# Kernel optimization log

Measured on AMD Instinct MI355X. Metric: run time of the kernel, lower is better.

The kernel has to match this reference:

```python
import jax, jax.numpy as jnp
import numpy as np

D = 1024
H = 16
HD = D // H
SCALE = HD ** -0.5


def setup_inputs() -> dict:
    key = jax.random.key(0)
    ks = jax.random.split(key, 5)
    x = jax.random.normal(ks[0], (2, 2048, D), dtype=jnp.float32)
    s = 1.0 / np.sqrt(D)
    W_qkv = jax.random.uniform(ks[1], (D, 3 * D), jnp.float32, -s, s)
    b_qkv = jax.random.uniform(ks[2], (3 * D,), jnp.float32, -s, s)
    W_out = jax.random.uniform(ks[3], (D, D), jnp.float32, -s, s)
    b_out = jax.random.uniform(ks[4], (D,), jnp.float32, -s, s)
    return {"x": x, "W_qkv": W_qkv, "b_qkv": b_qkv, "W_out": W_out, "b_out": b_out}


def reference(x, W_qkv, b_qkv, W_out, b_out):
    B, S, _ = x.shape
    qkv = x @ W_qkv + b_qkv                       # [B,S,3D]
    qkv = qkv.reshape(B, S, 3, H, HD)
    q, k, v = jnp.moveaxis(qkv, 2, 0)             # each [B,S,H,HD]
    # scores: [B,H,S,S]
    scores = jnp.einsum("bshd,bthd->bhst", q, k) * SCALE
    attn = jax.nn.softmax(scores, axis=-1)        # dropout is identity in eval mode
    out = jnp.einsum("bhst,bthd->bshd", attn, v)  # [B,S,H,HD]
    out = out.reshape(B, S, H * HD)
    return out @ W_out + b_out
```

## Files before the change

### kernel.cpp

```cpp
#include <hip/hip_runtime.h>

typedef unsigned short u16;
typedef unsigned int   u32;

using short8 = __attribute__((ext_vector_type(8))) short;
using f32x4  = __attribute__((ext_vector_type(4))) float;
using half4  = __attribute__((ext_vector_type(4))) _Float16;
using half8  = __attribute__((ext_vector_type(8))) _Float16;

#define QSCALE 0.18033688011112042f
#define SXR(r) ((((r) ^ ((r) >> 2))) & 3)

__device__ __forceinline__ u16 f2bf(float f) {
  u32 u = __float_as_uint(f);
  return (u16)((u + 0x8000u) >> 16);
}
__device__ __forceinline__ u16 f2h(float f) {
  _Float16 h = (_Float16)f;
  return __builtin_bit_cast(u16, h);
}

__device__ __forceinline__ void gld16(const u16* g, u16* l) {
  __builtin_amdgcn_global_load_lds(
      (const __attribute__((address_space(1))) unsigned int*)g,
      (__attribute__((address_space(3))) unsigned int*)l, 16, 0, 0);
}

__global__ __launch_bounds__(256) void prep(
    const float* __restrict__ x, u16* __restrict__ x_bf,
    const float* __restrict__ Wq, u16* __restrict__ wq_t,
    const float* __restrict__ Wo, u16* __restrict__ wo_t) {
  __shared__ u32 s[32][33];
  const int bid = blockIdx.x, tid = threadIdx.x;
  if (bid < 4096) {
    int idx = bid * 256 + tid;
    float4 v = reinterpret_cast<const float4*>(x)[idx];
    ushort4 o;
    o.x = f2bf(v.x); o.y = f2bf(v.y); o.z = f2bf(v.z); o.w = f2bf(v.w);
    reinterpret_cast<ushort4*>(x_bf)[idx] = o;
    return;
  }
  const float* in; u16* out; int R, C, bx, by;
  if (bid < 7168) { int b = bid - 4096; in = Wq; out = wq_t; R = 1024; C = 3072; bx = b % 96; by = b / 96; }
  else            { int b = bid - 7168; in = Wo; out = wo_t; R = 1024; C = 1024; bx = b % 32; by = b / 32; }
  int c0 = bx * 32, r0 = by * 32;
  int j = tid & 31, i0 = tid >> 5;
#pragma unroll
  for (int p = 0; p < 4; ++p) {
    int i = i0 + p * 8;
    s[i][j] = f2bf(in[(size_t)(r0 + i) * C + c0 + j]);
  }
  __syncthreads();
#pragma unroll
  for (int p = 0; p < 4; ++p) {
    int jj = i0 + p * 8;
    out[(size_t)(c0 + jj) * R + r0 + j] = (u16)s[j][jj];
  }
}

__global__ __launch_bounds__(256, 2) void gemm_qkv(
    const u16* __restrict__ A, const u16* __restrict__ Bt,
    const float* __restrict__ bias,
    u16* __restrict__ q_out, u16* __restrict__ k_out, u16* __restrict__ vt_out) {
  const int K = 1024;
  __shared__ __align__(16) u16 As[4][128 * 32];
  __shared__ __align__(16) u16 Bs[4][192 * 32];
  const int tid = threadIdx.x;
  const int lane = tid & 63, wv = tid >> 6;
  const int l16 = lane & 15, quad = lane >> 4;
  const int wm = wv & 1, wn = wv >> 1;

  const int lin = blockIdx.y * 16 + blockIdx.x;
  const int xcd = lin & 7, idx = lin >> 3;
  const int bx = (xcd & 1) * 8 + (idx & 7);
  const int by = (xcd >> 1) * 8 + (idx >> 3);

  const u16* Ab = A + (size_t)by * 128 * K;
  const u16* Bb = Bt + (size_t)bx * 192 * K;

  const int iA0 = tid, iA1 = 256 + tid;
  const int iB0 = tid, iB1 = 256 + tid, iB2 = 512 + tid;
  const u16* sA0 = Ab + (size_t)(iA0 >> 2) * K + (((iA0 & 3) ^ SXR(iA0 >> 2)) << 3);
  const u16* sA1 = Ab + (size_t)(iA1 >> 2) * K + (((iA1 & 3) ^ SXR(iA1 >> 2)) << 3);
  const u16* sB0 = Bb + (size_t)(iB0 >> 2) * K + (((iB0 & 3) ^ SXR(iB0 >> 2)) << 3);
  const u16* sB1 = Bb + (size_t)(iB1 >> 2) * K + (((iB1 & 3) ^ SXR(iB1 >> 2)) << 3);
  const u16* sB2 = Bb + (size_t)(iB2 >> 2) * K + (((iB2 & 3) ^ SXR(iB2 >> 2)) << 3);
  const int dA0 = iA0 << 3, dA1 = iA1 << 3;
  const int dB0 = iB0 << 3, dB1 = iB1 << 3, dB2 = iB2 << 3;

  int aoff[4], boff[6];
#pragma unroll
  for (int mi = 0; mi < 4; ++mi) {
    int r = wm * 64 + mi * 16 + l16;
    aoff[mi] = r * 32 + ((quad ^ SXR(r)) << 3);
  }
#pragma unroll
  for (int ni = 0; ni < 6; ++ni) {
    int r = wn * 96 + ni * 16 + l16;
    boff[ni] = r * 32 + ((quad ^ SXR(r)) << 3);
  }

  const f32x4 fzero = {0.0f, 0.0f, 0.0f, 0.0f};
  f32x4 acc[4][6];
#pragma unroll
  for (int i = 0; i < 4; ++i)
#pragma unroll
    for (int j = 0; j < 6; ++j) acc[i][j] = fzero;

#define STAGE_A(T)                        \
  do {                                    \
    gld16(sA0, &As[T][dA0]);              \
    gld16(sA1, &As[T][dA1]);              \
    sA0 += 32; sA1 += 32;                 \
  } while (0)
#define STAGE_B(T)                        \
  do {                                    \
    gld16(sB0, &Bs[T][dB0]);              \
    gld16(sB1, &Bs[T][dB1]);              \
    gld16(sB2, &Bs[T][dB2]);              \
    sB0 += 32; sB1 += 32; sB2 += 32;      \
  } while (0)
#define VM5 asm volatile("s_waitcnt vmcnt(5)" ::: "memory")
#define VM0 asm volatile("s_waitcnt vmcnt(0)" ::: "memory")

#define GTILE(S, T, DOST, VW)                                              \
  do {                                                                     \
    short8 bb[6];                                                          \
    _Pragma("unroll")                                                      \
    for (int j = 0; j < 6; ++j)                                            \
      bb[j] = *reinterpret_cast<const short8*>(&Bs[S][boff[j]]);           \
    short8 a0 = *reinterpret_cast<const short8*>(&As[S][aoff[0]]);         \
    short8 a1 = *reinterpret_cast<const short8*>(&As[S][aoff[1]]);         \
    short8 a2 = *reinterpret_cast<const short8*>(&As[S][aoff[2]]);         \
    short8 a3 = *reinterpret_cast<const short8*>(&As[S][aoff[3]]);         \
    if (DOST) { STAGE_A(T); STAGE_B(T); }                                  \
    __builtin_amdgcn_s_setprio(1);                                         \
    _Pragma("unroll")                                                      \
    for (int j = 0; j < 6; ++j) {                                          \
      acc[0][j] = __builtin_amdgcn_mfma_f32_16x16x32_bf16(a0, bb[j], acc[0][j], 0, 0, 0); \
      acc[1][j] = __builtin_amdgcn_mfma_f32_16x16x32_bf16(a1, bb[j], acc[1][j], 0, 0, 0); \
      acc[2][j] = __builtin_amdgcn_mfma_f32_16x16x32_bf16(a2, bb[j], acc[2][j], 0, 0, 0); \
      acc[3][j] = __builtin_amdgcn_mfma_f32_16x16x32_bf16(a3, bb[j], acc[3][j], 0, 0, 0); \
    }                                                                      \
    __builtin_amdgcn_s_setprio(0);                                         \
    VW;                                                                    \
    __builtin_amdgcn_s_barrier();                                          \
  } while (0)

  STAGE_A(0); STAGE_B(0);
  STAGE_A(1); STAGE_B(1);
  VM5;
  __builtin_amdgcn_s_barrier();

  for (int kb = 0; kb < 28; kb += 4) {
    GTILE(0, 2, 1, VM5);
    GTILE(1, 3, 1, VM5);
    GTILE(2, 0, 1, VM5);
    GTILE(3, 1, 1, VM5);
  }
  GTILE(0, 2, 1, VM5);
  GTILE(1, 3, 1, VM5);
  GTILE(2, 0, 0, VM0);
  GTILE(3, 1, 0, ((void)0));
#undef GTILE
#undef STAGE_A
#undef STAGE_B

#pragma unroll
  for (int mi = 0; mi < 4; ++mi)
#pragma unroll
    for (int ni = 0; ni < 6; ++ni) {
      int col = bx * 192 + wn * 96 + ni * 16 + l16;
      float bv = bias[col];
      int row0 = by * 128 + wm * 64 + mi * 16 + quad * 4;
      int which = col >> 10, rem = col & 1023;
      int h = rem >> 6, d = rem & 63;
      int b = row0 >> 11, sq0 = row0 & 2047;
      int bh = (b << 4) + h;
      if (which == 2) {
        ushort4 pk;
        pk.x = f2h(acc[mi][ni][0] + bv);
        pk.y = f2h(acc[mi][ni][1] + bv);
        pk.z = f2h(acc[mi][ni][2] + bv);
        pk.w = f2h(acc[mi][ni][3] + bv);
        size_t off = (size_t)bh * 131072 +
                     (((sq0 >> 2) * 16 + (d & 15)) * 16 + ((d >> 4) << 2));
        *reinterpret_cast<ushort4*>(&vt_out[off]) = pk;
      } else {
        size_t base = (size_t)(bh * 2048 + sq0) * 64 + d;
#pragma unroll
        for (int r = 0; r < 4; ++r) {
          float val = acc[mi][ni][r] + bv;
          if (which == 0) q_out[base + r * 64] = f2bf(val * QSCALE);
          else            k_out[base + r * 64] = f2bf(val);
        }
      }
    }
}

__global__ __launch_bounds__(256, 2) void gemm_op(
    const u16* __restrict__ A, const u16* __restrict__ Bt,
    const float* __restrict__ bias, float* __restrict__ c_out) {
  const int K = 1024;
  __shared__ __align__(16) u16 As[4][128 * 32];
  __shared__ __align__(16) u16 Bs[4][64 * 32];
  const int tid = threadIdx.x;
  const int lane = tid & 63, wv = tid >> 6;
  const int l16 = lane & 15, quad = lane >> 4;
  const int wm = wv & 1, wn = wv >> 1;

  const int lin = blockIdx.y * 16 + blockIdx.x;
  const int xcd = lin & 7, idx = lin >> 3;
  const int bx = (xcd & 1) * 8 + (idx & 7);
  const int by = (xcd >> 1) * 8 + (idx >> 3);

  const u16* Ab = A + (size_t)by * 128 * K;
  const u16* Bb = Bt + (size_t)bx * 64 * K;

  const int iA0 = tid, iA1 = 256 + tid, iB0 = tid;
  const u16* sA0 = Ab + (size_t)(iA0 >> 2) * K + (((iA0 & 3) ^ SXR(iA0 >> 2)) << 3);
  const u16* sA1 = Ab + (size_t)(iA1 >> 2) * K + (((iA1 & 3) ^ SXR(iA1 >> 2)) << 3);
  const u16* sB0 = Bb + (size_t)(iB0 >> 2) * K + (((iB0 & 3) ^ SXR(iB0 >> 2)) << 3);
  const int dA0 = iA0 << 3, dA1 = iA1 << 3, dB0 = iB0 << 3;

  int aoff[4], boff[2];
#pragma unroll
  for (int mi = 0; mi < 4; ++mi) {
    int r = wm * 64 + mi * 16 + l16;
    aoff[mi] = r * 32 + ((quad ^ SXR(r)) << 3);
  }
#pragma unroll
  for (int ni = 0; ni < 2; ++ni) {
    int r = wn * 32 + ni * 16 + l16;
    boff[ni] = r * 32 + ((quad ^ SXR(r)) << 3);
  }

  const f32x4 fzero = {0.0f, 0.0f, 0.0f, 0.0f};
  f32x4 acc[4][2];
#pragma unroll
  for (int i = 0; i < 4; ++i)
#pragma unroll
    for (int j = 0; j < 2; ++j) acc[i][j] = fzero;

#define STAGE_A(T)                        \
  do {                                    \
    gld16(sA0, &As[T][dA0]);              \
    gld16(sA1, &As[T][dA1]);              \
    sA0 += 32; sA1 += 32;                 \
  } while (0)
#define STAGE_B(T)                        \
  do {                                    \
    gld16(sB0, &Bs[T][dB0]);              \
    sB0 += 32;                            \
  } while (0)
#define VM3 asm volatile("s_waitcnt vmcnt(3)" ::: "memory")
#define VM0b asm volatile("s_waitcnt vmcnt(0)" ::: "memory")

#define OTILE(S, T, DOST, VW)                                              \
  do {                                                                     \
    short8 b0 = *reinterpret_cast<const short8*>(&Bs[S][boff[0]]);         \
    short8 b1 = *reinterpret_cast<const short8*>(&Bs[S][boff[1]]);         \
    short8 a0 = *reinterpret_cast<const short8*>(&As[S][aoff[0]]);         \
    short8 a1 = *reinterpret_cast<const short8*>(&As[S][aoff[1]]);         \
    short8 a2 = *reinterpret_cast<const short8*>(&As[S][aoff[2]]);         \
    short8 a3 = *reinterpret_cast<const short8*>(&As[S][aoff[3]]);         \
    if (DOST) { STAGE_A(T); STAGE_B(T); }                                  \
    __builtin_amdgcn_s_setprio(1);                                         \
    acc[0][0] = __builtin_amdgcn_mfma_f32_16x16x32_bf16(a0, b0, acc[0][0], 0, 0, 0); \
    acc[0][1] = __builtin_amdgcn_mfma_f32_16x16x32_bf16(a0, b1, acc[0][1], 0, 0, 0); \
    acc[1][0] = __builtin_amdgcn_mfma_f32_16x16x32_bf16(a1, b0, acc[1][0], 0, 0, 0); \
    acc[1][1] = __builtin_amdgcn_mfma_f32_16x16x32_bf16(a1, b1, acc[1][1], 0, 0, 0); \
    acc[2][0] = __builtin_amdgcn_mfma_f32_16x16x32_bf16(a2, b0, acc[2][0], 0, 0, 0); \
    acc[2][1] = __builtin_amdgcn_mfma_f32_16x16x32_bf16(a2, b1, acc[2][1], 0, 0, 0); \
    acc[3][0] = __builtin_amdgcn_mfma_f32_16x16x32_bf16(a3, b0, acc[3][0], 0, 0, 0); \
    acc[3][1] = __builtin_amdgcn_mfma_f32_16x16x32_bf16(a3, b1, acc[3][1], 0, 0, 0); \
    __builtin_amdgcn_s_setprio(0);                                         \
    VW;                                                                    \
    __builtin_amdgcn_s_barrier();                                          \
  } while (0)

  STAGE_A(0); STAGE_B(0);
  STAGE_A(1); STAGE_B(1);
  VM3;
  __builtin_amdgcn_s_barrier();

  for (int kb = 0; kb < 28; kb += 4) {
    OTILE(0, 2, 1, VM3);
    OTILE(1, 3, 1, VM3);
    OTILE(2, 0, 1, VM3);
    OTILE(3, 1, 1, VM3);
  }
  OTILE(0, 2, 1, VM3);
  OTILE(1, 3, 1, VM3);
  OTILE(2, 0, 0, VM0b);
  OTILE(3, 1, 0, ((void)0));
#undef OTILE
#undef STAGE_A
#undef STAGE_B

#pragma unroll
  for (int mi = 0; mi < 4; ++mi)
#pragma unroll
    for (int ni = 0; ni < 2; ++ni) {
      int col = bx * 64 + wn * 32 + ni * 16 + l16;
      float bv = bias[col];
      int row0 = by * 128 + wm * 64 + mi * 16 + quad * 4;
#pragma unroll
      for (int r = 0; r < 4; ++r)
        c_out[(size_t)(row0 + r) * 1024 + col] = acc[mi][ni][r] + bv;
    }
}

__global__ __launch_bounds__(256, 4) void attn(
    const u16* __restrict__ q_buf, const u16* __restrict__ k_buf,
    const u16* __restrict__ vt_buf, u16* __restrict__ o_buf) {
  __shared__ __align__(16) u16 Ks[2][4096];
  __shared__ __align__(16) u16 Vs[2][4096];

  const int tid = threadIdx.x;
  const int lane = tid & 63, w = tid >> 6;
  const int l16 = lane & 15, quad = lane >> 4;
  const int bh = blockIdx.x, q0 = blockIdx.y * 64;

  const u16* qg = q_buf + (size_t)bh * 131072 + (q0 + w * 16) * 64;
  const u16* kg = k_buf + (size_t)bh * 131072;
  const u16* vg = vt_buf + (size_t)bh * 131072;

  short8 qb[2];
#pragma unroll
  for (int kk = 0; kk < 2; ++kk)
    qb[kk] = *reinterpret_cast<const short8*>(qg + l16 * 64 + kk * 32 + quad * 8);

  const int idA = tid, idB = 256 + tid;
  const u16* ksA = kg + (idA >> 3) * 64 + (((idA & 7) ^ ((idA >> 3) & 7)) << 3);
  const u16* ksB = kg + (idB >> 3) * 64 + (((idB & 7) ^ ((idB >> 3) & 7)) << 3);
  const u16* vsA = vg + ((idA ^ ((idA >> 4) & 1)) << 3);
  const u16* vsB = vg + ((idB ^ ((idB >> 4) & 1)) << 3);
  const int ldA = idA << 3, ldB = idB << 3;

  int k0o[4], k1o[4], v0o[4], v1o[4];
#pragma unroll
  for (int t = 0; t < 4; ++t) {
    int rr = t * 16 + l16;
    k0o[t] = rr * 64 + ((quad ^ (rr & 7)) << 3);
    k1o[t] = rr * 64 + (((4 + quad) ^ (rr & 7)) << 3);
    int gb = (t * 4 + quad) * 32 + l16 * 2;
    int sw = (l16 >> 3) & 1;
    v0o[t] = (gb + sw) << 3;
    v1o[t] = (gb + (sw ^ 1)) << 3;
  }

  const f32x4 fzero = {0.0f, 0.0f, 0.0f, 0.0f};
  f32x4 o_acc[4];
  float l_acc = 0.f;
#pragma unroll
  for (int nd = 0; nd < 4; ++nd) o_acc[nd] = fzero;

#define STAGE(BUF)                           \
  do {                                       \
    gld16(ksA, &Ks[BUF][ldA]);               \
    gld16(ksB, &Ks[BUF][ldB]);               \
    gld16(vsA, &Vs[BUF][ldA]);               \
    gld16(vsB, &Vs[BUF][ldB]);               \
    ksA += 4096; ksB += 4096;                \
    vsA += 4096; vsB += 4096;                \
  } while (0)

#define TILE(BUF)                                                         \
  do {                                                                    \
    _Pragma("unroll")                                                     \
    for (int t = 0; t < 4; ++t) {                                         \
      short8 k0f = *reinterpret_cast<const short8*>(&Ks[BUF][k0o[t]]);    \
      short8 k1f = *reinterpret_cast<const short8*>(&Ks[BUF][k1o[t]]);    \
      half8 v0 = *reinterpret_cast<const half8*>(&Vs[BUF][v0o[t]]);       \
      half8 v1 = *reinterpret_cast<const half8*>(&Vs[BUF][v1o[t]]);       \
      half4 vb0 = __builtin_shufflevector(v0, v0, 0, 1, 2, 3);            \
      half4 vb1 = __builtin_shufflevector(v0, v0, 4, 5, 6, 7);            \
      half4 vb2 = __builtin_shufflevector(v1, v1, 0, 1, 2, 3);            \
      half4 vb3 = __builtin_shufflevector(v1, v1, 4, 5, 6, 7);            \
      __builtin_amdgcn_s_setprio(1);                                      \
      f32x4 s = __builtin_amdgcn_mfma_f32_16x16x32_bf16(k0f, qb[0], fzero, 0, 0, 0); \
      s = __builtin_amdgcn_mfma_f32_16x16x32_bf16(k1f, qb[1], s, 0, 0, 0);\
      __builtin_amdgcn_s_setprio(0);                                      \
      float p0 = __builtin_amdgcn_exp2f(s[0]);                            \
      float p1 = __builtin_amdgcn_exp2f(s[1]);                            \
      float p2 = __builtin_amdgcn_exp2f(s[2]);                            \
      float p3 = __builtin_amdgcn_exp2f(s[3]);                            \
      l_acc += (p0 + p1) + (p2 + p3);                                     \
      half4 pa;                                                           \
      pa[0] = (_Float16)p0; pa[1] = (_Float16)p1;                         \
      pa[2] = (_Float16)p2; pa[3] = (_Float16)p3;                         \
      __builtin_amdgcn_s_setprio(1);                                      \
      o_acc[0] = __builtin_amdgcn_mfma_f32_16x16x16f16(pa, vb0, o_acc[0], 0, 0, 0); \
      o_acc[1] = __builtin_amdgcn_mfma_f32_16x16x16f16(pa, vb1, o_acc[1], 0, 0, 0); \
      o_acc[2] = __builtin_amdgcn_mfma_f32_16x16x16f16(pa, vb2, o_acc[2], 0, 0, 0); \
      o_acc[3] = __builtin_amdgcn_mfma_f32_16x16x16f16(pa, vb3, o_acc[3], 0, 0, 0); \
      __builtin_amdgcn_s_setprio(0);                                      \
    }                                                                     \
  } while (0)

  STAGE(0);
  __syncthreads();

  for (int i = 0; i < 32; i += 2) {
    if (i + 1 < 32) STAGE(1);
    TILE(0);
    __syncthreads();
    if (i + 2 < 32) STAGE(0);
    TILE(1);
    __syncthreads();
  }
#undef STAGE
#undef TILE

  l_acc += __shfl_xor(l_acc, 16, 64);
  l_acc += __shfl_xor(l_acc, 32, 64);

  const int b = bh >> 4, h = bh & 15;
  float lv[4];
#pragma unroll
  for (int r = 0; r < 4; ++r)
    lv[r] = __shfl(l_acc, quad * 4 + r, 64);
#pragma unroll
  for (int nd = 0; nd < 4; ++nd) {
#pragma unroll
    for (int r = 0; r < 4; ++r) {
      int sq = q0 + w * 16 + quad * 4 + r;
      o_buf[(size_t)(b * 2048 + sq) * 1024 + h * 64 + nd * 16 + l16] =
          f2bf(o_acc[nd][r] / lv[r]);
    }
  }
}

extern "C" void kernel_launch(void* const* d_in, const int* in_sizes, int n_in,
                              void* d_out, int out_size, void* d_ws, size_t ws_size,
                              hipStream_t stream) {
  (void)in_sizes; (void)n_in; (void)out_size; (void)ws_size;
  const float* x     = (const float*)d_in[0];
  const float* W_qkv = (const float*)d_in[1];
  const float* b_qkv = (const float*)d_in[2];
  const float* W_out = (const float*)d_in[3];
  const float* b_out = (const float*)d_in[4];
  float* out = (float*)d_out;

  char* ws = (char*)d_ws;
  u16* x_bf   = (u16*)(ws);
  u16* wqkv_t = (u16*)(ws + 8388608);
  u16* wout_t = (u16*)(ws + 14680064);
  u16* q_buf  = (u16*)(ws + 16777216);
  u16* k_buf  = (u16*)(ws + 25165824);
  u16* vt_buf = (u16*)(ws + 33554432);
  u16* o_bf   = (u16*)(ws + 41943040);

  prep<<<8192, 256, 0, stream>>>(x, x_bf, W_qkv, wqkv_t, W_out, wout_t);
  gemm_qkv<<<dim3(16, 32), 256, 0, stream>>>(x_bf, wqkv_t, b_qkv,
                                             q_buf, k_buf, vt_buf);
  attn<<<dim3(32, 32), 256, 0, stream>>>(q_buf, k_buf, vt_buf, o_bf);
  gemm_op<<<dim3(16, 32), 256, 0, stream>>>(o_bf, wout_t, b_out, out);
}
```

Measured before the change: 181.8 us.

## Restructure QKV GEMM to 8 waves with double-buffered LDS

The QKV GEMM block grows from 256 to 512 threads, so each of eight waves computes a 64x48 sub-tile instead of 64x96, which halves the accumulator registers per wave. The 4-stage LDS ring with fine-grained vmcnt waits is replaced by a simpler 2-stage double buffer synchronized with __syncthreads. The goal is more waves per CU to hide latency, at the cost of shallower prefetch and heavier block-wide barriers. Only 256 of the 512 threads load the second B chunk.

```diff
diff --git a/kernel.cpp b/kernel.cpp
--- a/kernel.cpp
+++ b/kernel.cpp
@@ -58,13 +58,13 @@
   }
 }
 
-__global__ __launch_bounds__(256, 2) void gemm_qkv(
+__global__ __launch_bounds__(512, 4) void gemm_qkv(
     const u16* __restrict__ A, const u16* __restrict__ Bt,
     const float* __restrict__ bias,
     u16* __restrict__ q_out, u16* __restrict__ k_out, u16* __restrict__ vt_out) {
   const int K = 1024;
-  __shared__ __align__(16) u16 As[4][128 * 32];
-  __shared__ __align__(16) u16 Bs[4][192 * 32];
+  __shared__ __align__(16) u16 As[2][128 * 32];
+  __shared__ __align__(16) u16 Bs[2][192 * 32];
   const int tid = threadIdx.x;
   const int lane = tid & 63, wv = tid >> 6;
   const int l16 = lane & 15, quad = lane >> 4;
@@ -78,99 +78,83 @@
   const u16* Ab = A + (size_t)by * 128 * K;
   const u16* Bb = Bt + (size_t)bx * 192 * K;
 
-  const int iA0 = tid, iA1 = 256 + tid;
-  const int iB0 = tid, iB1 = 256 + tid, iB2 = 512 + tid;
-  const u16* sA0 = Ab + (size_t)(iA0 >> 2) * K + (((iA0 & 3) ^ SXR(iA0 >> 2)) << 3);
-  const u16* sA1 = Ab + (size_t)(iA1 >> 2) * K + (((iA1 & 3) ^ SXR(iA1 >> 2)) << 3);
-  const u16* sB0 = Bb + (size_t)(iB0 >> 2) * K + (((iB0 & 3) ^ SXR(iB0 >> 2)) << 3);
+  const int iB1 = 512 + tid;
+  const u16* sA  = Ab + (size_t)(tid >> 2) * K + (((tid & 3) ^ SXR(tid >> 2)) << 3);
+  const u16* sB0 = Bb + (size_t)(tid >> 2) * K + (((tid & 3) ^ SXR(tid >> 2)) << 3);
   const u16* sB1 = Bb + (size_t)(iB1 >> 2) * K + (((iB1 & 3) ^ SXR(iB1 >> 2)) << 3);
-  const u16* sB2 = Bb + (size_t)(iB2 >> 2) * K + (((iB2 & 3) ^ SXR(iB2 >> 2)) << 3);
-  const int dA0 = iA0 << 3, dA1 = iA1 << 3;
-  const int dB0 = iB0 << 3, dB1 = iB1 << 3, dB2 = iB2 << 3;
-
-  int aoff[4], boff[6];
+  const int dA = tid << 3, dB0 = tid << 3, dB1 = iB1 << 3;
+  const bool hasB1 = (tid < 256);
+
+  int aoff[4], boff[3];
 #pragma unroll
   for (int mi = 0; mi < 4; ++mi) {
     int r = wm * 64 + mi * 16 + l16;
     aoff[mi] = r * 32 + ((quad ^ SXR(r)) << 3);
   }
 #pragma unroll
-  for (int ni = 0; ni < 6; ++ni) {
-    int r = wn * 96 + ni * 16 + l16;
+  for (int ni = 0; ni < 3; ++ni) {
+    int r = wn * 48 + ni * 16 + l16;
     boff[ni] = r * 32 + ((quad ^ SXR(r)) << 3);
   }
 
   const f32x4 fzero = {0.0f, 0.0f, 0.0f, 0.0f};
-  f32x4 acc[4][6];
+  f32x4 acc[4][3];
 #pragma unroll
   for (int i = 0; i < 4; ++i)
 #pragma unroll
-    for (int j = 0; j < 6; ++j) acc[i][j] = fzero;
-
-#define STAGE_A(T)                        \
-  do {                                    \
-    gld16(sA0, &As[T][dA0]);              \
-    gld16(sA1, &As[T][dA1]);              \
-    sA0 += 32; sA1 += 32;                 \
-  } while (0)
-#define STAGE_B(T)                        \
-  do {                                    \
-    gld16(sB0, &Bs[T][dB0]);              \
-    gld16(sB1, &Bs[T][dB1]);              \
-    gld16(sB2, &Bs[T][dB2]);              \
-    sB0 += 32; sB1 += 32; sB2 += 32;      \
-  } while (0)
-#define VM5 asm volatile("s_waitcnt vmcnt(5)" ::: "memory")
-#define VM0 asm volatile("s_waitcnt vmcnt(0)" ::: "memory")
-
-#define GTILE(S, T, DOST, VW)                                              \
+    for (int j = 0; j < 3; ++j) acc[i][j] = fzero;
+
+#define STAGE(T)                              \
+  do {                                        \
+    gld16(sA, &As[T][dA]);   sA += 32;        \
+    gld16(sB0, &Bs[T][dB0]); sB0 += 32;       \
+    if (hasB1) { gld16(sB1, &Bs[T][dB1]); sB1 += 32; } \
+  } while (0)
+
+#define GTILE(S)                                                           \
   do {                                                                     \
-    short8 bb[6];                                                          \
-    _Pragma("unroll")                                                      \
-    for (int j = 0; j < 6; ++j)                                            \
-      bb[j] = *reinterpret_cast<const short8*>(&Bs[S][boff[j]]);           \
+    short8 b0 = *reinterpret_cast<const short8*>(&Bs[S][boff[0]]);         \
+    short8 b1 = *reinterpret_cast<const short8*>(&Bs[S][boff[1]]);         \
+    short8 b2 = *reinterpret_cast<const short8*>(&Bs[S][boff[2]]);         \
     short8 a0 = *reinterpret_cast<const short8*>(&As[S][aoff[0]]);         \
     short8 a1 = *reinterpret_cast<const short8*>(&As[S][aoff[1]]);         \
     short8 a2 = *reinterpret_cast<const short8*>(&As[S][aoff[2]]);         \
     short8 a3 = *reinterpret_cast<const short8*>(&As[S][aoff[3]]);         \
-    if (DOST) { STAGE_A(T); STAGE_B(T); }                                  \
     __builtin_amdgcn_s_setprio(1);                                         \
-    _Pragma("unroll")                                                      \
-    for (int j = 0; j < 6; ++j) {                                          \
-      acc[0][j] = __builtin_amdgcn_mfma_f32_16x16x32_bf16(a0, bb[j], acc[0][j], 0, 0, 0); \
-      acc[1][j] = __builtin_amdgcn_mfma_f32_16x16x32_bf16(a1, bb[j], acc[1][j], 0, 0, 0); \
-      acc[2][j] = __builtin_amdgcn_mfma_f32_16x16x32_bf16(a2, bb[j], acc[2][j], 0, 0, 0); \
-      acc[3][j] = __builtin_amdgcn_mfma_f32_16x16x32_bf16(a3, bb[j], acc[3][j], 0, 0, 0); \
-    }                                                                      \
+    acc[0][0] = __builtin_amdgcn_mfma_f32_16x16x32_bf16(a0, b0, acc[0][0], 0, 0, 0); \
+    acc[0][1] = __builtin_amdgcn_mfma_f32_16x16x32_bf16(a0, b1, acc[0][1], 0, 0, 0); \
+    acc[0][2] = __builtin_amdgcn_mfma_f32_16x16x32_bf16(a0, b2, acc[0][2], 0, 0, 0); \
+    acc[1][0] = __builtin_amdgcn_mfma_f32_16x16x32_bf16(a1, b0, acc[1][0], 0, 0, 0); \
+    acc[1][1] = __builtin_amdgcn_mfma_f32_16x16x32_bf16(a1, b1, acc[1][1], 0, 0, 0); \
+    acc[1][2] = __builtin_amdgcn_mfma_f32_16x16x32_bf16(a1, b2, acc[1][2], 0, 0, 0); \
+    acc[2][0] = __builtin_amdgcn_mfma_f32_16x16x32_bf16(a2, b0, acc[2][0], 0, 0, 0); \
+    acc[2][1] = __builtin_amdgcn_mfma_f32_16x16x32_bf16(a2, b1, acc[2][1], 0, 0, 0); \
+    acc[2][2] = __builtin_amdgcn_mfma_f32_16x16x32_bf16(a2, b2, acc[2][2], 0, 0, 0); \
+    acc[3][0] = __builtin_amdgcn_mfma_f32_16x16x32_bf16(a3, b0, acc[3][0], 0, 0, 0); \
+    acc[3][1] = __builtin_amdgcn_mfma_f32_16x16x32_bf16(a3, b1, acc[3][1], 0, 0, 0); \
+    acc[3][2] = __builtin_amdgcn_mfma_f32_16x16x32_bf16(a3, b2, acc[3][2], 0, 0, 0); \
     __builtin_amdgcn_s_setprio(0);                                         \
-    VW;                                                                    \
-    __builtin_amdgcn_s_barrier();                                          \
-  } while (0)
-
-  STAGE_A(0); STAGE_B(0);
-  STAGE_A(1); STAGE_B(1);
-  VM5;
-  __builtin_amdgcn_s_barrier();
-
-  for (int kb = 0; kb < 28; kb += 4) {
-    GTILE(0, 2, 1, VM5);
-    GTILE(1, 3, 1, VM5);
-    GTILE(2, 0, 1, VM5);
-    GTILE(3, 1, 1, VM5);
-  }
-  GTILE(0, 2, 1, VM5);
-  GTILE(1, 3, 1, VM5);
-  GTILE(2, 0, 0, VM0);
-  GTILE(3, 1, 0, ((void)0));
+  } while (0)
+
+  STAGE(0);
+  __syncthreads();
+
+  for (int i = 0; i < 32; i += 2) {
+    STAGE(1);
+    GTILE(0);
+    __syncthreads();
+    if (i + 2 < 32) STAGE(0);
+    GTILE(1);
+    __syncthreads();
+  }
 #undef GTILE
-#undef STAGE_A
-#undef STAGE_B
+#undef STAGE
 
 #pragma unroll
   for (int mi = 0; mi < 4; ++mi)
 #pragma unroll
-    for (int ni = 0; ni < 6; ++ni) {
-      int col = bx * 192 + wn * 96 + ni * 16 + l16;
+    for (int ni = 0; ni < 3; ++ni) {
+      int col = bx * 192 + wn * 48 + ni * 16 + l16;
       float bv = bias[col];
       int row0 = by * 128 + wm * 64 + mi * 16 + quad * 4;
       int which = col >> 10, rem = col & 1023;
@@ -453,7 +437,7 @@
   u16* o_bf   = (u16*)(ws + 41943040);
 
   prep<<<8192, 256, 0, stream>>>(x, x_bf, W_qkv, wqkv_t, W_out, wout_t);
-  gemm_qkv<<<dim3(16, 32), 256, 0, stream>>>(x_bf, wqkv_t, b_qkv,
+  gemm_qkv<<<dim3(16, 32), 512, 0, stream>>>(x_bf, wqkv_t, b_qkv,
                                              q_buf, k_buf, vt_buf);
   attn<<<dim3(32, 32), 256, 0, stream>>>(q_buf, k_buf, vt_buf, o_bf);
   gemm_op<<<dim3(16, 32), 256, 0, stream>>>(o_bf, wout_t, b_out, out);
```

Measured after the change: 185.1 us. No clear change (+1.8%).
